# Kernel optimization log

Hardware: AMD Instinct MI355X
Metric: run time of the kernel (lower is better)

## Reference

```python
import jax, jax.numpy as jnp
import numpy as np

N_NODES = 100000
N_EDGES = 1600000
F_IN = 64
HEADS = 2
D_HEAD = 64  # hidden_channels per head
F_OUT = HEADS * D_HEAD  # 128 (concat=True)
NEG_SLOPE = 0.2


def setup_inputs() -> dict:
    key = jax.random.key(0)
    ks = jax.random.split(key, 10)
    x = jax.random.normal(ks[0], (N_NODES, F_IN), dtype=jnp.float32)
    edge_index = jax.random.randint(ks[1], (2, N_EDGES), 0, N_NODES, dtype=jnp.int32)
    perm = jax.random.permutation(ks[2], N_NODES).astype(jnp.int32)
    s = 0.05
    W_src = jax.random.normal(ks[3], (F_IN, F_OUT), dtype=jnp.float32) * s
    W_dst = jax.random.normal(ks[4], (F_IN, F_OUT), dtype=jnp.float32) * s
    a_src = jax.random.normal(ks[5], (HEADS, D_HEAD), dtype=jnp.float32) * s
    a_dst = jax.random.normal(ks[6], (HEADS, D_HEAD), dtype=jnp.float32) * s
    bias = jnp.zeros((F_OUT,), dtype=jnp.float32)
    prelu_w = jnp.full((F_OUT,), 0.25, dtype=jnp.float32)  # torch PReLU default init
    return {"x": x, "edge_index": edge_index, "perm": perm,
            "W_src": W_src, "W_dst": W_dst, "a_src": a_src, "a_dst": a_dst,
            "bias": bias, "prelu_w": prelu_w}


def _gat_prelu(x, edge_index, W_src, W_dst, a_src, a_dst, bias, prelu_w):
    # PyG GATConv, add_self_loops=False, heads=HEADS, concat=True, then PReLU.
    N = x.shape[0]
    src, dst = edge_index[0], edge_index[1]
    xs = (x @ W_src).reshape(N, HEADS, D_HEAD)  # source-side projection
    xd = (x @ W_dst).reshape(N, HEADS, D_HEAD)  # destination-side projection
    al_s = jnp.einsum('nhd,hd->nh', xs, a_src)  # [N,H]
    al_d = jnp.einsum('nhd,hd->nh', xd, a_dst)  # [N,H]
    e = jax.nn.leaky_relu(al_s[src] + al_d[dst], NEG_SLOPE)  # [E,H]
    # softmax over incoming edges of each destination node
    m = jax.ops.segment_max(e, dst, num_segments=N)  # [N,H]
    ex = jnp.exp(e - m[dst])
    den = jax.ops.segment_sum(ex, dst, num_segments=N)  # [N,H]
    alpha = ex / (den[dst] + 1e-16)  # [E,H]
    msg = xs[src] * alpha[:, :, None]  # [E,H,D]
    out = jax.ops.segment_sum(msg, dst, num_segments=N)  # [N,H,D]
    out = out.reshape(N, F_OUT) + bias
    return jnp.where(out >= 0, out, prelu_w * out)


def reference(x, edge_index, perm, W_src, W_dst, a_src, a_dst, bias, prelu_w):
    # DGI forward: positive embedding, corrupted (negative) embedding, summary
    pos_z = _gat_prelu(x, edge_index, W_src, W_dst, a_src, a_dst, bias, prelu_w)
    x_cor = x[perm]  # corruption: permute node features, keep edges
    neg_z = _gat_prelu(x_cor, edge_index, W_src, W_dst, a_src, a_dst, bias, prelu_w)
    summary = jax.nn.sigmoid(pos_z.mean(axis=0))
    return pos_z, neg_z, summary
```

## Files before the change

### kernel.cpp

```cpp
#include <hip/hip_runtime.h>
#include <hip/hip_bf16.h>

#define F_IN   64
#define HEADS  2
#define D_HEAD 64
#define F_OUT  128
#define NEG_SLOPE 0.2f

#define AGG_GRID 2048
#define CAP 48

__global__ void zero_i(int* __restrict__ p, int n) {
    int i = blockIdx.x * blockDim.x + threadIdx.x;
    int step = gridDim.x * blockDim.x;
    for (; i < n; i += step) p[i] = 0;
}

__global__ void prep_kernel(const float* __restrict__ Ws, const float* __restrict__ Wd,
                            const float* __restrict__ as_, const float* __restrict__ ad_,
                            float* __restrict__ a2s, float* __restrict__ a2d) {
    int t = threadIdx.x;
    int k = t >> 1, h = t & 1;
    float ss = 0.f, sd = 0.f;
    for (int j = 0; j < 64; ++j) {
        ss += Ws[k * 128 + h * 64 + j] * as_[h * 64 + j];
        sd += Wd[k * 128 + h * 64 + j] * ad_[h * 64 + j];
    }
    a2s[t] = ss;
    a2d[t] = sd;
}

__global__ __launch_bounds__(256) void proj_kernel(
    const float* __restrict__ x, const float* __restrict__ W,
    const float* __restrict__ a2s, const float* __restrict__ a2d,
    __hip_bfloat16* __restrict__ xsb, float* __restrict__ als, float* __restrict__ ald, int N)
{
    __shared__ float Wsh[64 * 128];
    __shared__ float xsh[2][64];
    __shared__ float a2ssh[128], a2dsh[128];
    int t = threadIdx.x;
    for (int i = t; i < 64 * 128; i += 256) Wsh[i] = W[i];
    if (t < 128) { a2ssh[t] = a2s[t]; a2dsh[t] = a2d[t]; }
    __syncthreads();

    int slot = t >> 7;
    int c    = t & 127;
    int h    = c >> 6;
    int j    = c & 63;

    for (long long base = (long long)blockIdx.x * 2; base < N; base += (long long)gridDim.x * 2) {
        long long n = base + slot;
        __syncthreads();
        if (t < 128) {
            int sl = t >> 6, k = t & 63;
            long long nn = base + sl;
            xsh[sl][k] = (nn < N) ? x[nn * 64 + k] : 0.f;
        }
        __syncthreads();

        float acc = 0.f;
        #pragma unroll
        for (int k = 0; k < 64; ++k) acc += xsh[slot][k] * Wsh[k * 128 + c];

        float xv = xsh[slot][j];
        float rs = xv * a2ssh[j * 2 + h];
        float rd = xv * a2dsh[j * 2 + h];
        #pragma unroll
        for (int off = 32; off; off >>= 1) {
            rs += __shfl_down(rs, off, 64);
            rd += __shfl_down(rd, off, 64);
        }
        if (n < N) {
            xsb[n * 128 + c] = __float2bfloat16(acc);
            if (j == 0) {
                als[n * 2 + h] = rs;
                ald[n * 2 + h] = rd;
            }
        }
    }
}

__global__ void scatter_kernel(const int* __restrict__ src, const int* __restrict__ dst,
                               const int* __restrict__ perm,
                               int* __restrict__ cnt, int* __restrict__ csr,
                               int* __restrict__ csrp, int E) {
    int e = blockIdx.x * blockDim.x + threadIdx.x;
    if (e >= E) return;
    int s = src[e], d = dst[e];
    int slot = atomicAdd(&cnt[d], 1);
    if (slot < CAP) {
        csr [d * CAP + slot] = s;
        csrp[d * CAP + slot] = perm[s];
    }
}

__global__ __launch_bounds__(256) void aggfused_kernel(
    const int* __restrict__ cnt,
    const int* __restrict__ csrP, const int* __restrict__ csrN,
    const int* __restrict__ perm,
    const float* __restrict__ als, const float* __restrict__ ald,
    const unsigned* __restrict__ xsu,
    const float* __restrict__ bias, const float* __restrict__ pw,
    float* __restrict__ zP, float* __restrict__ zN,
    float* __restrict__ colsum, int N)
{
    int t    = threadIdx.x;
    int wid  = t >> 6;
    int lane = t & 63;
    int col  = lane * 2;
    int h    = lane >> 5;
    int rel  = lane & 31;
    float bi0 = bias[col], bi1 = bias[col + 1];
    float pw0 = pw[col],   pw1 = pw[col + 1];
    float sum0 = 0.f, sum1 = 0.f;

    for (int n = blockIdx.x * 4 + wid; n < N; n += AGG_GRID * 4) {
        int e0 = n * CAP;
        int e1 = e0 + min(cnt[n], CAP);
        float aldvP = ald[n * 2 + h];
        float aldvN = ald[perm[n] * 2 + h];
        float mP = -INFINITY, denP = 0.f, aP0 = 0.f, aP1 = 0.f;
        float mN = -INFINITY, denN = 0.f, aN0 = 0.f, aN1 = 0.f;

        for (int cb = e0; cb < e1; cb += 32) {
            int idx = cb + rel;
            bool valid = idx < e1;
            int idxc = valid ? idx : e0;
            int spP = csrP[idxc];
            int spN = csrN[idxc];
            float scP = als[spP * 2 + h] + aldvP;
            float scN = als[spN * 2 + h] + aldvN;
            scP = (scP >= 0.f) ? scP : NEG_SLOPE * scP;
            scN = (scN >= 0.f) ? scN : NEG_SLOPE * scN;
            if (!valid) { scP = -INFINITY; scN = -INFINITY; }

            float cmP = scP, cmN = scN;
            #pragma unroll
            for (int off = 16; off; off >>= 1) {
                cmP = fmaxf(cmP, __shfl_xor(cmP, off, 64));
                cmN = fmaxf(cmN, __shfl_xor(cmN, off, 64));
            }
            float mnP = fmaxf(mP, cmP), mnN = fmaxf(mN, cmN);
            float rP = __expf(mP - mnP), rN = __expf(mN - mnN);
            float wP = __expf(scP - mnP), wN = __expf(scN - mnN);
            float wsP = wP, wsN = wN;
            #pragma unroll
            for (int off = 16; off; off >>= 1) {
                wsP += __shfl_xor(wsP, off, 64);
                wsN += __shfl_xor(wsN, off, 64);
            }
            aP0 *= rP; aP1 *= rP; denP = denP * rP + wsP; mP = mnP;
            aN0 *= rN; aN1 *= rN; denN = denN * rN + wsN; mN = mnN;

            int ec = min(32, e1 - cb);
            int hb = h << 5;
            for (int i = 0; i < ec; i += 8) {
                float wp_[8], wn_[8]; int pp_[8], pn_[8]; unsigned vp_[8], vn_[8];
                #pragma unroll
                for (int k = 0; k < 8; ++k) {
                    wp_[k] = __shfl(wP, hb + i + k, 64);
                    pp_[k] = __shfl(spP, i + k, 64);
                    wn_[k] = __shfl(wN, hb + i + k, 64);
                    pn_[k] = __shfl(spN, i + k, 64);
                }
                #pragma unroll
                for (int k = 0; k < 8; ++k) {
                    vp_[k] = xsu[pp_[k] * 64 + lane];
                    vn_[k] = xsu[pn_[k] * 64 + lane];
                }
                #pragma unroll
                for (int k = 0; k < 8; ++k) {
                    float fp0 = __uint_as_float((vp_[k] & 0xffffu) << 16);
                    float fp1 = __uint_as_float(vp_[k] & 0xffff0000u);
                    aP0 += wp_[k] * fp0;
                    aP1 += wp_[k] * fp1;
                    float fn0 = __uint_as_float((vn_[k] & 0xffffu) << 16);
                    float fn1 = __uint_as_float(vn_[k] & 0xffff0000u);
                    aN0 += wn_[k] * fn0;
                    aN1 += wn_[k] * fn1;
                }
            }
        }

        float inv = 1.f / (denP + 1e-16f);
        float v0 = aP0 * inv + bi0;
        float v1 = aP1 * inv + bi1;
        v0 = (v0 >= 0.f) ? v0 : pw0 * v0;
        v1 = (v1 >= 0.f) ? v1 : pw1 * v1;
        *reinterpret_cast<float2*>(zP + (long long)n * 128 + col) = make_float2(v0, v1);
        sum0 += v0; sum1 += v1;

        inv = 1.f / (denN + 1e-16f);
        v0 = aN0 * inv + bi0;
        v1 = aN1 * inv + bi1;
        v0 = (v0 >= 0.f) ? v0 : pw0 * v0;
        v1 = (v1 >= 0.f) ? v1 : pw1 * v1;
        *reinterpret_cast<float2*>(zN + (long long)n * 128 + col) = make_float2(v0, v1);
    }

    __shared__ float sh[512];
    sh[t * 2]     = sum0;
    sh[t * 2 + 1] = sum1;
    __syncthreads();
    if (wid == 0) {
        float s0 = sh[t * 2]     + sh[(t + 64) * 2]     + sh[(t + 128) * 2]     + sh[(t + 192) * 2];
        float s1 = sh[t * 2 + 1] + sh[(t + 64) * 2 + 1] + sh[(t + 128) * 2 + 1] + sh[(t + 192) * 2 + 1];
        atomicAdd(&colsum[col],     s0);
        atomicAdd(&colsum[col + 1], s1);
    }
}

__global__ void summary_kernel(const float* __restrict__ colsum, float* __restrict__ out,
                               float invN)
{
    int c = threadIdx.x;
    float m = colsum[c] * invN;
    out[c] = 1.f / (1.f + expf(-m));
}

extern "C" void kernel_launch(void* const* d_in, const int* in_sizes, int n_in,
                              void* d_out, int out_size, void* d_ws, size_t ws_size,
                              hipStream_t stream) {
    const float* x      = (const float*)d_in[0];
    const int*   ei     = (const int*)  d_in[1];
    const int*   perm   = (const int*)  d_in[2];
    const float* Wsrc   = (const float*)d_in[3];
    const float* Wdst   = (const float*)d_in[4];
    const float* a_src  = (const float*)d_in[5];
    const float* a_dst  = (const float*)d_in[6];
    const float* bias   = (const float*)d_in[7];
    const float* prelu  = (const float*)d_in[8];

    const int N = in_sizes[0] / F_IN;
    const int E = in_sizes[1] / 2;
    const int* src = ei;
    const int* dst = ei + E;

    float* ws = (float*)d_ws;
    long long off = 0;
    float* a2s    = ws + off; off += 128;
    float* a2d    = ws + off; off += 128;
    float* als    = ws + off; off += 2LL * N;
    float* ald    = ws + off; off += 2LL * N;
    int*   cnt    = (int*)(ws + off); off += N;
    float* colsum = ws + off; off += 128;
    int*   csr    = (int*)(ws + off); off += (long long)N * CAP;
    int*   csrp   = (int*)(ws + off); off += (long long)N * CAP;
    unsigned* xsu = (unsigned*)(ws + off); off += (long long)N * 64;

    float* outP = (float*)d_out;
    float* outN = outP + (long long)N * F_OUT;
    float* outS = outN + (long long)N * F_OUT;

    prep_kernel<<<1, 128, 0, stream>>>(Wsrc, Wdst, a_src, a_dst, a2s, a2d);
    proj_kernel<<<1024, 256, 0, stream>>>(x, Wsrc, a2s, a2d, (__hip_bfloat16*)xsu, als, ald, N);

    zero_i<<<256, 256, 0, stream>>>(cnt, N + 128);
    const int eb = (E + 255) / 256;
    scatter_kernel<<<eb, 256, 0, stream>>>(src, dst, perm, cnt, csr, csrp, E);

    aggfused_kernel<<<AGG_GRID, 256, 0, stream>>>(cnt, csr, csrp, perm, als, ald, xsu,
                                                  bias, prelu, outP, outN, colsum, N);

    summary_kernel<<<1, 128, 0, stream>>>(colsum, outS, 1.0f / (float)N);
}
```

Measured before the change: 428.6 us.

## Fuse prep and zeroing into projection, interleave CSR pairs, deepen gather unroll

Removes the separate prep and zero kernels by computing the attention-vector folding and zeroing the counters inside the projection kernel. Stores positive and corrupted source indices as interleaved int2 pairs so the aggregation loads them together. Widens the feature gather batch from 8 to 16 edges and moves the weight shuffles into the accumulate loop. This saves launches and raises memory-level parallelism, at the cost of more registers and redundant per-block prep work.

```diff
diff --git a/kernel.cpp b/kernel.cpp
--- a/kernel.cpp
+++ b/kernel.cpp
@@ -10,38 +10,34 @@
 #define AGG_GRID 2048
 #define CAP 48
 
-__global__ void zero_i(int* __restrict__ p, int n) {
-    int i = blockIdx.x * blockDim.x + threadIdx.x;
-    int step = gridDim.x * blockDim.x;
-    for (; i < n; i += step) p[i] = 0;
-}
-
-__global__ void prep_kernel(const float* __restrict__ Ws, const float* __restrict__ Wd,
-                            const float* __restrict__ as_, const float* __restrict__ ad_,
-                            float* __restrict__ a2s, float* __restrict__ a2d) {
-    int t = threadIdx.x;
-    int k = t >> 1, h = t & 1;
-    float ss = 0.f, sd = 0.f;
-    for (int j = 0; j < 64; ++j) {
-        ss += Ws[k * 128 + h * 64 + j] * as_[h * 64 + j];
-        sd += Wd[k * 128 + h * 64 + j] * ad_[h * 64 + j];
-    }
-    a2s[t] = ss;
-    a2d[t] = sd;
-}
-
 __global__ __launch_bounds__(256) void proj_kernel(
     const float* __restrict__ x, const float* __restrict__ W,
-    const float* __restrict__ a2s, const float* __restrict__ a2d,
-    __hip_bfloat16* __restrict__ xsb, float* __restrict__ als, float* __restrict__ ald, int N)
+    const float* __restrict__ Wd,
+    const float* __restrict__ as_, const float* __restrict__ ad_,
+    __hip_bfloat16* __restrict__ xsb, float* __restrict__ als, float* __restrict__ ald,
+    int* __restrict__ cnt, int N)
 {
     __shared__ float Wsh[64 * 128];
     __shared__ float xsh[2][64];
     __shared__ float a2ssh[128], a2dsh[128];
     int t = threadIdx.x;
+
+    for (int g = blockIdx.x * 256 + t; g < N + 128; g += gridDim.x * 256) cnt[g] = 0;
+
     for (int i = t; i < 64 * 128; i += 256) Wsh[i] = W[i];
-    if (t < 128) { a2ssh[t] = a2s[t]; a2dsh[t] = a2d[t]; }
     __syncthreads();
+
+    if (t < 128) {
+        int k = t >> 1, hh = t & 1;
+        float ss = 0.f, sd = 0.f;
+        #pragma unroll 8
+        for (int j = 0; j < 64; ++j) {
+            ss += Wsh[k * 128 + hh * 64 + j] * as_[hh * 64 + j];
+            sd += Wd [k * 128 + hh * 64 + j] * ad_[hh * 64 + j];
+        }
+        a2ssh[t] = ss;
+        a2dsh[t] = sd;
+    }
 
     int slot = t >> 7;
     int c    = t & 127;
@@ -82,21 +78,17 @@
 
 __global__ void scatter_kernel(const int* __restrict__ src, const int* __restrict__ dst,
                                const int* __restrict__ perm,
-                               int* __restrict__ cnt, int* __restrict__ csr,
-                               int* __restrict__ csrp, int E) {
+                               int* __restrict__ cnt, int2* __restrict__ csr2, int E) {
     int e = blockIdx.x * blockDim.x + threadIdx.x;
     if (e >= E) return;
     int s = src[e], d = dst[e];
     int slot = atomicAdd(&cnt[d], 1);
-    if (slot < CAP) {
-        csr [d * CAP + slot] = s;
-        csrp[d * CAP + slot] = perm[s];
-    }
+    if (slot < CAP) csr2[d * CAP + slot] = make_int2(s, perm[s]);
 }
 
 __global__ __launch_bounds__(256) void aggfused_kernel(
     const int* __restrict__ cnt,
-    const int* __restrict__ csrP, const int* __restrict__ csrN,
+    const int2* __restrict__ csr2,
     const int* __restrict__ perm,
     const float* __restrict__ als, const float* __restrict__ ald,
     const unsigned* __restrict__ xsu,
@@ -126,8 +118,9 @@
             int idx = cb + rel;
             bool valid = idx < e1;
             int idxc = valid ? idx : e0;
-            int spP = csrP[idxc];
-            int spN = csrN[idxc];
+            int2 sp2 = csr2[idxc];
+            int spP = sp2.x;
+            int spN = sp2.y;
             float scP = als[spP * 2 + h] + aldvP;
             float scN = als[spN * 2 + h] + aldvN;
             scP = (scP >= 0.f) ? scP : NEG_SLOPE * scP;
@@ -154,30 +147,27 @@
 
             int ec = min(32, e1 - cb);
             int hb = h << 5;
-            for (int i = 0; i < ec; i += 8) {
-                float wp_[8], wn_[8]; int pp_[8], pn_[8]; unsigned vp_[8], vn_[8];
+            for (int i = 0; i < ec; i += 16) {
+                unsigned vp_[16], vn_[16];
                 #pragma unroll
-                for (int k = 0; k < 8; ++k) {
-                    wp_[k] = __shfl(wP, hb + i + k, 64);
-                    pp_[k] = __shfl(spP, i + k, 64);
-                    wn_[k] = __shfl(wN, hb + i + k, 64);
-                    pn_[k] = __shfl(spN, i + k, 64);
+                for (int k = 0; k < 16; ++k) {
+                    int pp = __shfl(spP, i + k, 64);
+                    vp_[k] = xsu[pp * 64 + lane];
+                    int pn = __shfl(spN, i + k, 64);
+                    vn_[k] = xsu[pn * 64 + lane];
                 }
                 #pragma unroll
-                for (int k = 0; k < 8; ++k) {
-                    vp_[k] = xsu[pp_[k] * 64 + lane];
-                    vn_[k] = xsu[pn_[k] * 64 + lane];
-                }
-                #pragma unroll
-                for (int k = 0; k < 8; ++k) {
+                for (int k = 0; k < 16; ++k) {
+                    float wp = __shfl(wP, hb + i + k, 64);
+                    float wn = __shfl(wN, hb + i + k, 64);
                     float fp0 = __uint_as_float((vp_[k] & 0xffffu) << 16);
                     float fp1 = __uint_as_float(vp_[k] & 0xffff0000u);
-                    aP0 += wp_[k] * fp0;
-                    aP1 += wp_[k] * fp1;
+                    aP0 += wp * fp0;
+                    aP1 += wp * fp1;
                     float fn0 = __uint_as_float((vn_[k] & 0xffffu) << 16);
                     float fn1 = __uint_as_float(vn_[k] & 0xffff0000u);
-                    aN0 += wn_[k] * fn0;
-                    aN1 += wn_[k] * fn1;
+                    aN0 += wn * fn0;
+                    aN1 += wn * fn1;
                 }
             }
         }
@@ -238,28 +228,24 @@
 
     float* ws = (float*)d_ws;
     long long off = 0;
-    float* a2s    = ws + off; off += 128;
-    float* a2d    = ws + off; off += 128;
     float* als    = ws + off; off += 2LL * N;
     float* ald    = ws + off; off += 2LL * N;
     int*   cnt    = (int*)(ws + off); off += N;
     float* colsum = ws + off; off += 128;
-    int*   csr    = (int*)(ws + off); off += (long long)N * CAP;
-    int*   csrp   = (int*)(ws + off); off += (long long)N * CAP;
+    int2*  csr2   = (int2*)(ws + off); off += 2LL * N * CAP;
     unsigned* xsu = (unsigned*)(ws + off); off += (long long)N * 64;
 
     float* outP = (float*)d_out;
     float* outN = outP + (long long)N * F_OUT;
     float* outS = outN + (long long)N * F_OUT;
 
-    prep_kernel<<<1, 128, 0, stream>>>(Wsrc, Wdst, a_src, a_dst, a2s, a2d);
-    proj_kernel<<<1024, 256, 0, stream>>>(x, Wsrc, a2s, a2d, (__hip_bfloat16*)xsu, als, ald, N);
-
-    zero_i<<<256, 256, 0, stream>>>(cnt, N + 128);
+    proj_kernel<<<1024, 256, 0, stream>>>(x, Wsrc, Wdst, a_src, a_dst,
+                                          (__hip_bfloat16*)xsu, als, ald, cnt, N);
+
     const int eb = (E + 255) / 256;
-    scatter_kernel<<<eb, 256, 0, stream>>>(src, dst, perm, cnt, csr, csrp, E);
-
-    aggfused_kernel<<<AGG_GRID, 256, 0, stream>>>(cnt, csr, csrp, perm, als, ald, xsu,
+    scatter_kernel<<<eb, 256, 0, stream>>>(src, dst, perm, cnt, csr2, E);
+
+    aggfused_kernel<<<AGG_GRID, 256, 0, stream>>>(cnt, csr2, perm, als, ald, xsu,
                                                   bias, prelu, outP, outN, colsum, N);
 
     summary_kernel<<<1, 128, 0, stream>>>(colsum, outS, 1.0f / (float)N);
```

Result: no change. 425.6 us (-0.7%).
